# Kernel tuning notes

Hardware: AMD Instinct MI355X
Metric: run time of the kernel (lower is better)

The kernel has to match this reference:

```python
import jax, jax.numpy as jnp
import numpy as np

# dims from init_kwargs
B, T = 64, 128
CB, DB = 8, 256
IN_DIM = CB + DB            # 264
H_STATE = 512
NUM_HEADS = 4
NUM_SHIFT = 3
M = 128                     # memory content size (slot width)
A = 2048                    # number of memory addresses
READ_SIZE = NUM_HEADS * M   # 512
PARAMS_PER_HEAD = M + 1 + 1 + NUM_SHIFT + 1 + 2 * M  # key,beta,g,shift,gamma,erase,add = 390
UPDATE_SIZE = NUM_HEADS * PARAMS_PER_HEAD             # 1560
EPS = 1e-8


def setup_inputs() -> dict:
    key = jax.random.key(0)
    ks = jax.random.split(key, 4)
    w = lambda k, sh: jax.random.normal(k, sh, jnp.float32) * 0.02
    return {
        "x": jax.random.normal(ks[0], (B, T, IN_DIM), jnp.float32),
        "W_state": w(ks[1], (IN_DIM + H_STATE + READ_SIZE, H_STATE)),
        "b_state": jnp.zeros((H_STATE,), jnp.float32),
        "W_out": w(ks[2], (H_STATE, DB)),
        "b_out": jnp.zeros((DB,), jnp.float32),
        "W_upd": w(ks[3], (H_STATE, UPDATE_SIZE)),
        "b_upd": jnp.zeros((UPDATE_SIZE,), jnp.float32),
    }


def _ntm_step(params, carry, x_t):
    W_state, b_state, W_out, b_out, W_upd, b_upd = params
    h, wt, mem = carry  # h [B,S], wt [B,H,A], mem [B,M,A]

    # --- read from memory with previous attention ---
    read = jnp.einsum('bma,bha->bhm', mem, wt).reshape(B, READ_SIZE)

    # --- controller ---
    ctrl_in = jnp.concatenate([x_t, h, read], axis=-1)
    h_new = jax.nn.sigmoid(ctrl_in @ W_state + b_state)
    out = jax.nn.sigmoid(h_new @ W_out + b_out)
    upd = (h_new @ W_upd + b_upd).reshape(B, NUM_HEADS, PARAMS_PER_HEAD)

    # --- split interface parameters per head ---
    k_vec = upd[..., :M]                                              # key [B,H,M]
    beta = jax.nn.softplus(upd[..., M:M + 1])                         # key strength
    g = jax.nn.sigmoid(upd[..., M + 1:M + 2])                         # interpolation gate
    shift = jax.nn.softmax(upd[..., M + 2:M + 2 + NUM_SHIFT], axis=-1)
    gamma = 1.0 + jax.nn.softplus(upd[..., M + 2 + NUM_SHIFT:M + 3 + NUM_SHIFT])
    erase = jax.nn.sigmoid(upd[..., M + 3 + NUM_SHIFT:2 * M + 3 + NUM_SHIFT])
    add = jnp.tanh(upd[..., 2 * M + 3 + NUM_SHIFT:])

    # --- content addressing: cosine similarity + sharpened softmax ---
    dots = jnp.einsum('bhm,bma->bha', k_vec, mem)
    k_norm = jnp.linalg.norm(k_vec, axis=-1, keepdims=True)           # [B,H,1]
    m_norm = jnp.linalg.norm(mem, axis=1)[:, None, :]                 # [B,1,A]
    sim = dots / (k_norm * m_norm + EPS)
    wc = jax.nn.softmax(beta * sim, axis=-1)

    # --- gate with previous attention ---
    wg = g * wc + (1.0 - g) * wt

    # --- circular convolutional shift (small fixed loop over NUM_SHIFT) ---
    center = NUM_SHIFT // 2
    shifted = jnp.stack([jnp.roll(wg, s - center, axis=-1) for s in range(NUM_SHIFT)], axis=2)  # [B,H,S,A]
    ws = jnp.einsum('bhs,bhsa->bha', shift, shifted)

    # --- sharpening ---
    wp = jnp.power(ws + EPS, gamma)
    wt_new = wp / jnp.sum(wp, axis=-1, keepdims=True)

    # --- memory erase / add ---
    erase_term = jnp.prod(1.0 - jnp.einsum('bhm,bha->bhma', erase, wt_new), axis=1)  # [B,M,A]
    add_term = jnp.einsum('bhm,bha->bma', add, wt_new)
    mem_new = mem * erase_term + add_term

    return (h_new, wt_new, mem_new), out


def reference(x, W_state, b_state, W_out, b_out, W_upd, b_upd):
    # init_state (matches torch module): h=ones, wt one-hot at address 0, mem=0.01
    h0 = jnp.ones((B, H_STATE), jnp.float32)
    wt0 = jnp.zeros((B, NUM_HEADS, A), jnp.float32).at[:, :, 0].set(1.0)
    mem0 = jnp.full((B, M, A), 0.01, jnp.float32)
    params = (W_state, b_state, W_out, b_out, W_upd, b_upd)

    def step(carry, x_t):
        return _ntm_step(params, carry, x_t)

    _, outs = jax.lax.scan(step, (h0, wt0, mem0), jnp.swapaxes(x, 0, 1))
    return jnp.swapaxes(outs, 0, 1)  # [B, T, DB]
```

## Files before the change

### kernel.cpp

```cpp
#include <hip/hip_runtime.h>
#include <math.h>

#define BB 64
#define TT 128
#define DBX 256
#define IND 264
#define HS 512
#define NH 4
#define MMM 128
#define AAA 2048
#define PPH 390
#define NCOLS (DBX + NH*PPH)
#define KTOT (IND + HS + HS)
#define KSPL 16
#define KCH  81
#define EPSF 1e-8f

__device__ __forceinline__ float sigmf(float x){ return 1.0f/(1.0f+expf(-x)); }
__device__ __forceinline__ float softplusf(float x){ return (x > 20.0f) ? x : log1pf(expf(x)); }

__global__ void k_init(float* __restrict__ hT, float* __restrict__ readT,
                       float* __restrict__ wt, float* __restrict__ mem){
  int i = blockIdx.x*blockDim.x + threadIdx.x;
  int stride = gridDim.x*blockDim.x;
  for (int idx=i; idx<BB*MMM*AAA; idx+=stride) mem[idx]=0.01f;
  for (int idx=i; idx<HS*BB; idx+=stride){ hT[idx]=1.0f; readT[idx]=0.01f; }
  for (int idx=i; idx<BB*NH*AAA; idx+=stride) wt[idx] = ((idx & (AAA-1))==0)?1.0f:0.0f;
}

__global__ __launch_bounds__(256) void k_tx(const float* __restrict__ x, float* __restrict__ xT){
  int b = blockIdx.x;
  for (int f = threadIdx.x; f < TT*IND; f += 256)
    xT[(size_t)f*BB + b] = x[(size_t)b*TT*IND + f];
}

__global__ __launch_bounds__(256) void k1_state(
    const float* __restrict__ xT, const float* __restrict__ Wst,
    const float* __restrict__ hTp, const float* __restrict__ readTp,
    float* __restrict__ hpart, float* __restrict__ wcsum, float* __restrict__ wpsum, int t)
{
  int tid = threadIdx.x, wave = tid>>6, lane = tid&63;
  int ks = blockIdx.y;
  int j0 = blockIdx.x*16 + wave*4;
  if (blockIdx.x==0 && ks==0){
    wcsum[tid] = 0.0f;
    wpsum[tid] = 0.0f;
  }
  float a0=0,a1=0,a2=0,a3=0;
  int k0 = ks*KCH, kend = k0+KCH;
  if (kend > KTOT) kend = KTOT;

  #define K1STEP(AEXPR) { float aV=(AEXPR); \
      float4 wv = *(const float4*)(Wst + (size_t)k*HS + j0); \
      a0 += aV*wv.x; a1 += aV*wv.y; a2 += aV*wv.z; a3 += aV*wv.w; }

  {int s = k0, e = kend<IND?kend:IND;
   #pragma unroll 4
   for (int k=s;k<e;++k) K1STEP(xT[((size_t)t*IND + k)*BB + lane]); }
  {int s = k0>IND?k0:IND, e = kend<(IND+HS)?kend:(IND+HS);
   #pragma unroll 4
   for (int k=s;k<e;++k) K1STEP(hTp[(k-IND)*BB + lane]); }
  {int s = k0>(IND+HS)?k0:(IND+HS), e = kend;
   #pragma unroll 4
   for (int k=s;k<e;++k) K1STEP(readTp[(k-IND-HS)*BB + lane]); }
  #undef K1STEP

  float* hp = hpart + (size_t)ks*HS*BB + (size_t)j0*BB + lane;
  hp[0]    = a0;
  hp[BB]   = a1;
  hp[2*BB] = a2;
  hp[3*BB] = a3;
}

__global__ __launch_bounds__(256) void k2h(
    const float* __restrict__ hpart, const float* __restrict__ bst, float* __restrict__ hTn)
{
  int idx = blockIdx.x*256 + threadIdx.x;
  float v = 0.0f;
  #pragma unroll
  for (int ks=0; ks<KSPL; ++ks) v += hpart[(size_t)ks*HS*BB + idx];
  hTn[idx] = sigmf(v + bst[idx>>6]);
}

__global__ __launch_bounds__(256) void k2_outupd(
    const float* __restrict__ hTn,
    const float* __restrict__ Wout, const float* __restrict__ bout,
    const float* __restrict__ Wupd, const float* __restrict__ bupd,
    float* __restrict__ out,
    float* __restrict__ kvec_t, float* __restrict__ beta, float* __restrict__ gbuf,
    float* __restrict__ gam, float* __restrict__ shraw,
    float* __restrict__ erase, float* __restrict__ addb, int t)
{
  __shared__ float part[4][4][BB];
  int tid = threadIdx.x, ks = tid>>6, lane = tid&63;
  int c0 = blockIdx.x*4;
  bool isout = (c0 < DBX);
  size_t strd = isout ? (size_t)DBX : (size_t)(NH*PPH);
  const float* wbase = isout ? (Wout + c0) : (Wupd + (c0 - DBX));

  float acc[4] = {0,0,0,0};
  {
    int k0 = ks*128;
    #pragma unroll 4
    for (int k=k0; k<k0+128; ++k){
      float a = hTn[k*BB + lane];
      float4 wa = *(const float4*)(wbase + (size_t)k*strd);
      acc[0]+=a*wa.x; acc[1]+=a*wa.y; acc[2]+=a*wa.z; acc[3]+=a*wa.w;
    }
  }
  #pragma unroll
  for (int u=0; u<4; ++u) part[ks][u][lane] = acc[u];
  __syncthreads();

  {
    int idx = tid;
    int u = idx>>6, b = idx&63;
    int c = c0+u;
    float v = part[0][u][b] + part[1][u][b] + part[2][u][b] + part[3][u][b];
    if (isout){
      out[((size_t)b*TT + t)*DBX + c] = sigmf(v + bout[c]);
    } else {
      int u2 = c - DBX;
      int hh = u2 / PPH;
      int p  = u2 - hh*PPH;
      v += bupd[u2];
      if (p < MMM)            kvec_t[b*HS + p*NH + hh] = v;
      else if (p == MMM)      beta[b*NH+hh] = softplusf(v);
      else if (p == MMM+1)    gbuf[b*NH+hh] = sigmf(v);
      else if (p <  MMM+5)    shraw[(b*NH+hh)*3 + (p-(MMM+2))] = v;
      else if (p == MMM+5)    gam[b*NH+hh] = 1.0f + softplusf(v);
      else if (p <  2*MMM+6)  erase[b*HS + hh*MMM + (p-(MMM+6))] = sigmf(v);
      else                    addb[b*HS + hh*MMM + (p-(2*MMM+6))] = tanhf(v);
    }
  }
}

__global__ __launch_bounds__(512) void k_dotsP(
    const float* __restrict__ mem, const float* __restrict__ kvec_t,
    float* __restrict__ dpart, float* __restrict__ n2part)
{
  int b = blockIdx.x, s = blockIdx.y, z = blockIdx.z, tid = threadIdx.x;
  __shared__ __align__(16) float klt[128];
  if (tid < 128) klt[tid] = kvec_t[b*HS + z*128 + tid];
  __syncthreads();
  int a = s*512 + tid;
  const float* mp = mem + (size_t)b*MMM*AAA + (size_t)(z*32)*AAA + a;
  const float4* k4 = (const float4*)klt;
  float a0=0,a1=0,a2=0,a3=0,n2=0;
  #pragma unroll 8
  for (int m=0; m<32; ++m){
    float mv = mp[(size_t)m*AAA];
    float4 kv = k4[m];
    a0 += kv.x*mv; a1 += kv.y*mv; a2 += kv.z*mv; a3 += kv.w*mv;
    n2 += mv*mv;
  }
  size_t base = ((size_t)(z*BB+b)*NH)*AAA + a;
  dpart[base]        = a0;
  dpart[base+AAA]    = a1;
  dpart[base+2*AAA]  = a2;
  dpart[base+3*AAA]  = a3;
  n2part[(size_t)(z*BB+b)*AAA + a] = n2;
}

__global__ __launch_bounds__(512) void k_dotsF(
    const float* __restrict__ dpart, const float* __restrict__ n2part,
    const float* __restrict__ kvec_t, const float* __restrict__ beta,
    float* __restrict__ ebuf, float* __restrict__ wcsum)
{
  int b = blockIdx.x, s = blockIdx.y, tid = threadIdx.x;
  __shared__ float red[HS];
  __shared__ float kn[NH];
  __shared__ float rsum[8*NH];
  float kv = kvec_t[b*HS + tid];
  red[tid] = kv*kv;
  __syncthreads();
  #pragma unroll
  for (int off=256; off>=4; off>>=1){
    if (tid < off) red[tid] += red[tid+off];
    __syncthreads();
  }
  if (tid < NH) kn[tid] = sqrtf(red[tid]);
  __syncthreads();

  int a = s*512 + tid;
  float d[NH] = {0,0,0,0};
  float n2 = 0.0f;
  #pragma unroll
  for (int z=0; z<4; ++z){
    size_t base = ((size_t)(z*BB+b)*NH)*AAA + a;
    d[0] += dpart[base];
    d[1] += dpart[base+AAA];
    d[2] += dpart[base+2*AAA];
    d[3] += dpart[base+3*AAA];
    n2   += n2part[(size_t)(z*BB+b)*AAA + a];
  }
  float mn = sqrtf(n2);
  int wid = tid >> 6, lane = tid & 63;
  #pragma unroll
  for (int hh=0; hh<NH; ++hh){
    float sim = d[hh]/(kn[hh]*mn + EPSF);
    float e = expf(beta[b*NH+hh]*sim);
    ebuf[((size_t)(b*NH+hh))*AAA + a] = e;
    float v = e;
    #pragma unroll
    for (int off=32; off>0; off>>=1) v += __shfl_xor(v, off);
    if (lane==0) rsum[wid*NH+hh] = v;
  }
  __syncthreads();
  if (tid < NH){
    float s2 = 0.0f;
    #pragma unroll
    for (int w=0; w<8; ++w) s2 += rsum[w*NH+tid];
    atomicAdd(&wcsum[b*NH+tid], s2);
  }
}

__global__ __launch_bounds__(512) void k_shift(
    const float* __restrict__ ebuf, const float* __restrict__ wcsum,
    const float* __restrict__ gbuf, const float* __restrict__ shraw,
    const float* __restrict__ gam, const float* __restrict__ wt,
    float* __restrict__ wpb, float* __restrict__ wpsum)
{
  int b = blockIdx.x, s = blockIdx.y, tid = threadIdx.x;
  int a = s*512 + tid;
  int am1 = (a + AAA - 1) & (AAA-1);
  int ap1 = (a + 1) & (AAA-1);
  __shared__ float sh[NH*3], gl[NH], gml[NH], winv[NH];
  __shared__ float rsum[8*NH];
  if (tid < NH){
    int hh = tid;
    float s0=shraw[(b*NH+hh)*3], s1=shraw[(b*NH+hh)*3+1], s2=shraw[(b*NH+hh)*3+2];
    float mx = fmaxf(s0, fmaxf(s1, s2));
    float e0=expf(s0-mx), e1=expf(s1-mx), e2=expf(s2-mx);
    float inv = 1.0f/(e0+e1+e2);
    sh[hh*3+0]=e0*inv; sh[hh*3+1]=e1*inv; sh[hh*3+2]=e2*inv;
    gl[hh]  = gbuf[b*NH+hh];
    gml[hh] = gam[b*NH+hh];
    winv[hh]= 1.0f/wcsum[b*NH+hh];
  }
  __syncthreads();
  int wid = tid >> 6, lane = tid & 63;
  #pragma unroll
  for (int hh=0; hh<NH; ++hh){
    const float* eb = ebuf + ((size_t)(b*NH+hh))*AAA;
    const float* wb = wt   + ((size_t)(b*NH+hh))*AAA;
    float inv = winv[hh], g = gl[hh];
    float s0 = sh[hh*3+0], s1 = sh[hh*3+1], s2 = sh[hh*3+2];
    float wgm1 = g*eb[am1]*inv + (1.0f-g)*wb[am1];
    float wg0  = g*eb[a]  *inv + (1.0f-g)*wb[a];
    float wgp1 = g*eb[ap1]*inv + (1.0f-g)*wb[ap1];
    float ws = s0*wgp1 + s1*wg0 + s2*wgm1;
    float wp = powf(ws + EPSF, gml[hh]);
    wpb[((size_t)(b*NH+hh))*AAA + a] = wp;
    float v = wp;
    #pragma unroll
    for (int off=32; off>0; off>>=1) v += __shfl_xor(v, off);
    if (lane==0) rsum[wid*NH+hh] = v;
  }
  __syncthreads();
  if (tid < NH){
    float s3 = 0.0f;
    #pragma unroll
    for (int w=0; w<8; ++w) s3 += rsum[w*NH+tid];
    atomicAdd(&wpsum[b*NH+tid], s3);
  }
}

__global__ __launch_bounds__(512) void k_updAB(
    float* __restrict__ mem, const float* __restrict__ wpb, const float* __restrict__ wpsum,
    const float* __restrict__ erase, const float* __restrict__ addb,
    float* __restrict__ wt, float* __restrict__ readTn)
{
  __shared__ __align__(16) float wl[AAA*4];
  int b = blockIdx.x, my = blockIdx.y, tid = threadIdx.x;
  int wave = tid >> 6, lane = tid & 63;
  float winv[4];
  #pragma unroll
  for (int h=0;h<4;++h) winv[h] = 1.0f/wpsum[b*NH+h];
  #pragma unroll
  for (int c4=0;c4<4;++c4){
    int a = c4*512 + tid;
    float w0 = wpb[((size_t)(b*NH+0))*AAA + a]*winv[0];
    float w1 = wpb[((size_t)(b*NH+1))*AAA + a]*winv[1];
    float w2 = wpb[((size_t)(b*NH+2))*AAA + a]*winv[2];
    float w3 = wpb[((size_t)(b*NH+3))*AAA + a]*winv[3];
    wl[a*4+0]=w0; wl[a*4+1]=w1; wl[a*4+2]=w2; wl[a*4+3]=w3;
    if (my == 0){
      wt[((size_t)(b*NH+0))*AAA + a] = w0;
      wt[((size_t)(b*NH+1))*AAA + a] = w1;
      wt[((size_t)(b*NH+2))*AAA + a] = w2;
      wt[((size_t)(b*NH+3))*AAA + a] = w3;
    }
  }
  __syncthreads();

  int m0 = my*8 + wave, m1 = m0 + 64;
  float er0[4], ad0[4], er1[4], ad1[4];
  #pragma unroll
  for (int h=0;h<4;++h){
    er0[h] = erase[b*HS + h*MMM + m0];
    ad0[h] = addb [b*HS + h*MMM + m0];
    er1[h] = erase[b*HS + h*MMM + m1];
    ad1[h] = addb [b*HS + h*MMM + m1];
  }
  float* row0 = mem + (size_t)b*MMM*AAA + (size_t)m0*AAA;
  float* row1 = mem + (size_t)b*MMM*AAA + (size_t)m1*AAA;
  const float4* wl4 = (const float4*)wl;
  float r00=0,r01=0,r02=0,r03=0, r10=0,r11=0,r12=0,r13=0;
  #pragma unroll 4
  for (int it=0; it<32; ++it){
    int a = it*64 + lane;
    float mv0 = row0[a], mv1 = row1[a];
    float4 w4 = wl4[a];
    float et0 = (1.0f - er0[0]*w4.x)*(1.0f - er0[1]*w4.y)
              * (1.0f - er0[2]*w4.z)*(1.0f - er0[3]*w4.w);
    float at0 = ad0[0]*w4.x + ad0[1]*w4.y + ad0[2]*w4.z + ad0[3]*w4.w;
    float n0 = mv0*et0 + at0;
    row0[a] = n0;
    r00 += n0*w4.x; r01 += n0*w4.y; r02 += n0*w4.z; r03 += n0*w4.w;
    float et1 = (1.0f - er1[0]*w4.x)*(1.0f - er1[1]*w4.y)
              * (1.0f - er1[2]*w4.z)*(1.0f - er1[3]*w4.w);
    float at1 = ad1[0]*w4.x + ad1[1]*w4.y + ad1[2]*w4.z + ad1[3]*w4.w;
    float n1 = mv1*et1 + at1;
    row1[a] = n1;
    r10 += n1*w4.x; r11 += n1*w4.y; r12 += n1*w4.z; r13 += n1*w4.w;
  }
  float rr[2][NH] = {{r00,r01,r02,r03},{r10,r11,r12,r13}};
  #pragma unroll
  for (int q=0; q<2; ++q){
    #pragma unroll
    for (int hh=0; hh<NH; ++hh){
      float v = rr[q][hh];
      #pragma unroll
      for (int off=32; off>0; off>>=1) v += __shfl_xor(v, off);
      rr[q][hh] = v;
    }
  }
  if (lane == 0){
    #pragma unroll
    for (int hh=0; hh<NH; ++hh){
      readTn[(size_t)(hh*MMM+m0)*BB + b] = rr[0][hh];
      readTn[(size_t)(hh*MMM+m1)*BB + b] = rr[1][hh];
    }
  }
}

extern "C" void kernel_launch(void* const* d_in, const int* in_sizes, int n_in,
                              void* d_out, int out_size, void* d_ws, size_t ws_size,
                              hipStream_t stream){
  const float* x    = (const float*)d_in[0];
  const float* Wst  = (const float*)d_in[1];
  const float* bst  = (const float*)d_in[2];
  const float* Wout = (const float*)d_in[3];
  const float* bout = (const float*)d_in[4];
  const float* Wupd = (const float*)d_in[5];
  const float* bupd = (const float*)d_in[6];
  float* out = (float*)d_out;

  float* p = (float*)d_ws;
  float* hT     = p; p += 2*HS*BB;
  float* readT  = p; p += 2*HS*BB;
  float* hpart  = p; p += KSPL*HS*BB;
  float* xT     = p; p += (size_t)TT*IND*BB;
  float* wt     = p; p += BB*NH*AAA;
  float* mem    = p; p += (size_t)BB*MMM*AAA;
  float* kvec_t = p; p += BB*HS;
  float* beta   = p; p += BB*NH;
  float* gbuf   = p; p += BB*NH;
  float* gam    = p; p += BB*NH;
  float* shraw  = p; p += BB*NH*3;
  float* erase  = p; p += BB*HS;
  float* addb   = p; p += BB*HS;
  float* ebuf   = p; p += BB*NH*AAA;
  float* wpb    = p; p += 4*(size_t)BB*NH*AAA;
  float* n2part = p; p += 4*BB*AAA;
  float* wcsum  = p; p += BB*NH;
  float* wpsum  = p; p += BB*NH;
  float* dpart  = wpb;

  k_init<<<2048, 256, 0, stream>>>(hT, readT, wt, mem);
  k_tx<<<BB, 256, 0, stream>>>(x, xT);
  for (int t=0; t<TT; ++t){
    const float* hTp = hT    + (t&1)*HS*BB;
    float* hTn       = hT    + ((t+1)&1)*HS*BB;
    const float* rTp = readT + (t&1)*HS*BB;
    float* rTn       = readT + ((t+1)&1)*HS*BB;
    k1_state<<<dim3(32,KSPL), 256, 0, stream>>>(xT, Wst, hTp, rTp, hpart, wcsum, wpsum, t);
    k2h<<<128, 256, 0, stream>>>(hpart, bst, hTn);
    k2_outupd<<<dim3(518), 256, 0, stream>>>(hTn, Wout, bout, Wupd, bupd, out,
        kvec_t, beta, gbuf, gam, shraw, erase, addb, t);
    k_dotsP<<<dim3(BB,4,4), 512, 0, stream>>>(mem, kvec_t, dpart, n2part);
    k_dotsF<<<dim3(BB,4), 512, 0, stream>>>(dpart, n2part, kvec_t, beta, ebuf, wcsum);
    k_shift<<<dim3(BB,4), 512, 0, stream>>>(ebuf, wcsum, gbuf, shraw, gam, wt, wpb, wpsum);
    k_updAB<<<dim3(BB,8), 512, 0, stream>>>(mem, wpb, wpsum, erase, addb, wt, rTn);
  }
}
```

Measured before the change: 9.775 ms.

## Fuse partial dot-product and finalize kernels into a single content-addressing kernel

Merges k_dotsP and k_dotsF into one kernel, k_dots. Each block splits the 128 memory rows between two 256-thread halves and combines their partial dot products and norms in shared memory, replacing the 4-way z-split that went through global memory. This removes the dpart/n2part global write and read-back and one kernel launch per timestep, and batches 16 memory loads per thread to raise memory-level parallelism. The cost is fewer blocks per launch, and half of each block's threads sit idle during the finalize stage.

```diff
diff --git a/kernel.cpp b/kernel.cpp
--- a/kernel.cpp
+++ b/kernel.cpp
@@ -135,44 +135,21 @@
   }
 }
 
-__global__ __launch_bounds__(512) void k_dotsP(
+__global__ __launch_bounds__(512) void k_dots(
     const float* __restrict__ mem, const float* __restrict__ kvec_t,
-    float* __restrict__ dpart, float* __restrict__ n2part)
-{
-  int b = blockIdx.x, s = blockIdx.y, z = blockIdx.z, tid = threadIdx.x;
-  __shared__ __align__(16) float klt[128];
-  if (tid < 128) klt[tid] = kvec_t[b*HS + z*128 + tid];
-  __syncthreads();
-  int a = s*512 + tid;
-  const float* mp = mem + (size_t)b*MMM*AAA + (size_t)(z*32)*AAA + a;
-  const float4* k4 = (const float4*)klt;
-  float a0=0,a1=0,a2=0,a3=0,n2=0;
-  #pragma unroll 8
-  for (int m=0; m<32; ++m){
-    float mv = mp[(size_t)m*AAA];
-    float4 kv = k4[m];
-    a0 += kv.x*mv; a1 += kv.y*mv; a2 += kv.z*mv; a3 += kv.w*mv;
-    n2 += mv*mv;
-  }
-  size_t base = ((size_t)(z*BB+b)*NH)*AAA + a;
-  dpart[base]        = a0;
-  dpart[base+AAA]    = a1;
-  dpart[base+2*AAA]  = a2;
-  dpart[base+3*AAA]  = a3;
-  n2part[(size_t)(z*BB+b)*AAA + a] = n2;
-}
-
-__global__ __launch_bounds__(512) void k_dotsF(
-    const float* __restrict__ dpart, const float* __restrict__ n2part,
-    const float* __restrict__ kvec_t, const float* __restrict__ beta,
+    const float* __restrict__ beta,
     float* __restrict__ ebuf, float* __restrict__ wcsum)
 {
   int b = blockIdx.x, s = blockIdx.y, tid = threadIdx.x;
-  __shared__ float red[HS];
-  __shared__ float kn[NH];
-  __shared__ float rsum[8*NH];
-  float kv = kvec_t[b*HS + tid];
-  red[tid] = kv*kv;
+  __shared__ __align__(16) float kl[HS];
+  __shared__ float red[512];
+  __shared__ float kn[NH], pb[NH];
+  __shared__ float comb[256*5];
+  __shared__ float rs[8*NH];
+  kl[tid] = kvec_t[b*HS + tid];
+  if (tid < NH) pb[tid] = beta[b*NH + tid];
+  __syncthreads();
+  red[tid] = kl[tid]*kl[tid];
   __syncthreads();
   #pragma unroll
   for (int off=256; off>=4; off>>=1){
@@ -182,35 +159,56 @@
   if (tid < NH) kn[tid] = sqrtf(red[tid]);
   __syncthreads();
 
-  int a = s*512 + tid;
-  float d[NH] = {0,0,0,0};
-  float n2 = 0.0f;
-  #pragma unroll
-  for (int z=0; z<4; ++z){
-    size_t base = ((size_t)(z*BB+b)*NH)*AAA + a;
-    d[0] += dpart[base];
-    d[1] += dpart[base+AAA];
-    d[2] += dpart[base+2*AAA];
-    d[3] += dpart[base+3*AAA];
-    n2   += n2part[(size_t)(z*BB+b)*AAA + a];
-  }
-  float mn = sqrtf(n2);
-  int wid = tid >> 6, lane = tid & 63;
+  int col = tid & 255;
+  int mh  = tid >> 8;
+  int a = s*256 + col;
+  const float* mp = mem + (size_t)b*MMM*AAA + (size_t)(mh*64)*AAA + a;
+  const float4* k4 = (const float4*)kl;
+  float d0=0,d1=0,d2=0,d3=0,n2=0;
+  for (int mb=0; mb<64; mb+=16){
+    float mv[16];
+    #pragma unroll
+    for (int u=0;u<16;++u) mv[u] = mp[(size_t)(mb+u)*AAA];
+    #pragma unroll
+    for (int u=0;u<16;++u){
+      float4 kv = k4[mh*64 + mb+u];
+      d0 += kv.x*mv[u]; d1 += kv.y*mv[u]; d2 += kv.z*mv[u]; d3 += kv.w*mv[u];
+      n2 += mv[u]*mv[u];
+    }
+  }
+  if (mh){
+    comb[col*5+0]=d0; comb[col*5+1]=d1; comb[col*5+2]=d2; comb[col*5+3]=d3; comb[col*5+4]=n2;
+  }
+  __syncthreads();
+  float e_r[NH];
+  if (!mh){
+    d0 += comb[col*5+0]; d1 += comb[col*5+1]; d2 += comb[col*5+2]; d3 += comb[col*5+3];
+    n2 += comb[col*5+4];
+    float mn = sqrtf(n2);
+    float dd[NH] = {d0,d1,d2,d3};
+    #pragma unroll
+    for (int hh=0; hh<NH; ++hh){
+      float sim = dd[hh]/(kn[hh]*mn + EPSF);
+      e_r[hh] = expf(pb[hh]*sim);
+      ebuf[((size_t)(b*NH+hh))*AAA + a] = e_r[hh];
+    }
+  } else {
+    #pragma unroll
+    for (int hh=0; hh<NH; ++hh) e_r[hh] = 0.0f;
+  }
+  int wave = tid >> 6, lane = tid & 63;
   #pragma unroll
   for (int hh=0; hh<NH; ++hh){
-    float sim = d[hh]/(kn[hh]*mn + EPSF);
-    float e = expf(beta[b*NH+hh]*sim);
-    ebuf[((size_t)(b*NH+hh))*AAA + a] = e;
-    float v = e;
+    float v = e_r[hh];
     #pragma unroll
     for (int off=32; off>0; off>>=1) v += __shfl_xor(v, off);
-    if (lane==0) rsum[wid*NH+hh] = v;
+    if (lane==0) rs[wave*NH+hh] = v;
   }
   __syncthreads();
   if (tid < NH){
     float s2 = 0.0f;
     #pragma unroll
-    for (int w=0; w<8; ++w) s2 += rsum[w*NH+tid];
+    for (int w=0; w<8; ++w) s2 += rs[w*NH+tid];
     atomicAdd(&wcsum[b*NH+tid], s2);
   }
 }
@@ -372,11 +370,9 @@
   float* erase  = p; p += BB*HS;
   float* addb   = p; p += BB*HS;
   float* ebuf   = p; p += BB*NH*AAA;
-  float* wpb    = p; p += 4*(size_t)BB*NH*AAA;
-  float* n2part = p; p += 4*BB*AAA;
+  float* wpb    = p; p += BB*NH*AAA;
   float* wcsum  = p; p += BB*NH;
   float* wpsum  = p; p += BB*NH;
-  float* dpart  = wpb;
 
   k_init<<<2048, 256, 0, stream>>>(hT, readT, wt, mem);
   k_tx<<<BB, 256, 0, stream>>>(x, xT);
@@ -389,8 +385,7 @@
     k2h<<<128, 256, 0, stream>>>(hpart, bst, hTn);
     k2_outupd<<<dim3(518), 256, 0, stream>>>(hTn, Wout, bout, Wupd, bupd, out,
         kvec_t, beta, gbuf, gam, shraw, erase, addb, t);
-    k_dotsP<<<dim3(BB,4,4), 512, 0, stream>>>(mem, kvec_t, dpart, n2part);
-    k_dotsF<<<dim3(BB,4), 512, 0, stream>>>(dpart, n2part, kvec_t, beta, ebuf, wcsum);
+    k_dots<<<dim3(BB,8), 512, 0, stream>>>(mem, kvec_t, beta, ebuf, wcsum);
     k_shift<<<dim3(BB,4), 512, 0, stream>>>(ebuf, wcsum, gbuf, shraw, gam, wt, wpb, wpsum);
     k_updAB<<<dim3(BB,8), 512, 0, stream>>>(mem, wpb, wpsum, erase, addb, wt, rTn);
   }
```

New measurement: 9.272 ms (median of 2 runs). -5.1%, faster.
